# Optimization experiments

Hardware: AMD Instinct MI355X
Metric: run time of the kernel (lower is better)

Reference implementation:

```python
import jax, jax.numpy as jnp
import numpy as np

LEVEL_NUM = 8  # init kwarg level_num (scale is unused by forward)


def setup_inputs() -> dict:
    key = jax.random.key(0)
    x = jax.random.normal(key, (1, 1024, 1024), dtype=jnp.float32)
    return {"x": x}


def reference(x):
    N, H, W = x.shape
    L = LEVEL_NUM
    q_levels = jnp.linspace(x.min(), x.max(), L)          # (L,)
    sigma = 2.0 / L                                        # 1 / (level_num/2)
    # soft quantization: (N,H,W,L)
    quant = jnp.exp(-((x[..., None] - q_levels) ** 2) / (sigma ** 2))
    quant = jnp.transpose(quant, (0, 3, 1, 2))             # (N,L,H,W)
    quant = jnp.pad(quant, ((0, 0), (0, 0), (0, 1), (0, 1)))  # (N,L,H+1,W+1)
    quant_left = quant[:, :, None, :H, :W]                 # (N,L,1,H,W)
    quant_right = quant[:, None, :, 1:, 1:]                # (N,1,L,H,W)
    co_occurrence = quant_left * quant_right               # (N,L,L,H,W)
    sta = co_occurrence.sum(axis=(-1, -2))                 # (N,L,L)
    sta = sta / sta.sum(axis=(1, 2))                       # valid since N==1
    # q_levels_h[n,i,j] = q_levels[j]; q_levels_w[n,i,j] = q_levels[i]
    q_h = jnp.broadcast_to(q_levels[None, None, :], (N, L, L))
    q_w = jnp.broadcast_to(q_levels[None, :, None], (N, L, L))
    output = jnp.stack([q_h, q_w, sta], axis=1).reshape(N, 3, L * L)[0]  # (3, L*L)
    return output, quant[0], co_occurrence[0]
```

## Files before the change

### kernel.cpp

```cpp
#include <hip/hip_runtime.h>

#define H 1024
#define W 1024
#define L 8
#define QH 1025
#define QW 1025
#define OUT0 192
#define QUANT_ELEMS (L * QH * QW)

#define CROWS 32
#define NCHUNK 32
#define BPC 72

#define WS_MIN 0
#define WS_MAX 16
#define WS_STA 32
#define WS_STRIDE 16
#define WS_SLOTS (WS_STA + 64 * WS_STRIDE)

__device__ __forceinline__ unsigned enc_ord(float f) {
    unsigned b = __float_as_uint(f);
    return (b & 0x80000000u) ? ~b : (b ^ 0x80000000u);
}
__device__ __forceinline__ float dec_ord(unsigned u) {
    unsigned b = (u & 0x80000000u) ? (u ^ 0x80000000u) : ~u;
    return __uint_as_float(b);
}
__device__ __forceinline__ float qlev(float mn, float step, float mx, int i) {
    return (i == L - 1) ? mx : mn + step * (float)i;
}

__global__ void k_init(unsigned* ws) {
    int t = threadIdx.x;
    for (int i = t; i < WS_SLOTS; i += 256)
        ws[i] = (i == WS_MIN) ? 0xFFFFFFFFu : 0u;
}

__global__ __launch_bounds__(256) void k_minmax(const float4* __restrict__ x4, unsigned* ws) {
    int t = threadIdx.x;
    int gid = blockIdx.x * 256 + t;
    float mn = 1e30f, mx = -1e30f;
    #pragma unroll
    for (int i = 0; i < 4; ++i) {
        float4 v = x4[gid + i * 65536];
        mn = fminf(mn, fminf(fminf(v.x, v.y), fminf(v.z, v.w)));
        mx = fmaxf(mx, fmaxf(fmaxf(v.x, v.y), fmaxf(v.z, v.w)));
    }
    #pragma unroll
    for (int m = 1; m < 64; m <<= 1) {
        mn = fminf(mn, __shfl_xor(mn, m, 64));
        mx = fmaxf(mx, __shfl_xor(mx, m, 64));
    }
    __shared__ float smn[4], smx[4];
    if ((t & 63) == 0) { smn[t >> 6] = mn; smx[t >> 6] = mx; }
    __syncthreads();
    if (t == 0) {
        mn = fminf(fminf(smn[0], smn[1]), fminf(smn[2], smn[3]));
        mx = fmaxf(fmaxf(smx[0], smx[1]), fmaxf(smx[2], smx[3]));
        atomicMin(&ws[WS_MIN], enc_ord(mn));
        atomicMax(&ws[WS_MAX], enc_ord(mx));
    }
}

__global__ __launch_bounds__(256) void k_main(const float* __restrict__ x,
                                              float* __restrict__ out,
                                              unsigned* __restrict__ ws) {
    const float mnv = dec_ord(ws[WS_MIN]);
    const float mxv = dec_ord(ws[WS_MAX]);
    const float step = (mxv - mnv) * (1.0f / 7.0f);

    float* __restrict__ quant = out + OUT0;
    float* __restrict__ co    = out + OUT0 + QUANT_ELEMS;

    const int bid = blockIdx.x;
    const int c = bid / BPC, k = bid - c * BPC;
    const int r0 = c * CROWS;
    const int t = threadIdx.x, w0 = t * 4;

    if (k < 64) {
        const int i = k >> 3, j = k & 7;
        const float qi = qlev(mnv, step, mxv, i);
        const float qj = qlev(mnv, step, mxv, j);
        float* cop = co + k * (H * W) + r0 * W + w0;
        float acc = 0.0f;

        for (int r = 0; r < CROWS; ++r) {
            const int h = r0 + r;
            float4 xl = *(const float4*)(x + h * W + w0);
            const bool hok = (h + 1 < H);
            float xr0 = 0.f, xr1 = 0.f, xr2 = 0.f, xr3 = 0.f;
            bool ok3 = false;
            if (hok) {
                float4 a = *(const float4*)(x + (h + 1) * W + w0);
                xr0 = a.y; xr1 = a.z; xr2 = a.w;
                ok3 = (w0 + 4 < W);
                if (ok3) xr3 = x[(h + 1) * W + w0 + 4];
            }
            float d;
            d = xl.x - qi; float l0 = __expf(-16.f * d * d);
            d = xl.y - qi; float l1 = __expf(-16.f * d * d);
            d = xl.z - qi; float l2 = __expf(-16.f * d * d);
            d = xl.w - qi; float l3 = __expf(-16.f * d * d);
            d = xr0 - qj; float p0 = hok ? __expf(-16.f * d * d) : 0.f;
            d = xr1 - qj; float p1 = hok ? __expf(-16.f * d * d) : 0.f;
            d = xr2 - qj; float p2 = hok ? __expf(-16.f * d * d) : 0.f;
            d = xr3 - qj; float p3 = (hok && ok3) ? __expf(-16.f * d * d) : 0.f;

            float4 v;
            v.x = l0 * p0; v.y = l1 * p1; v.z = l2 * p2; v.w = l3 * p3;
            *(float4*)cop = v;
            cop += W;
            acc += (v.x + v.y) + (v.z + v.w);
        }

        #pragma unroll
        for (int m = 1; m < 64; m <<= 1) acc += __shfl_xor(acc, m, 64);
        __shared__ float red[4];
        if ((t & 63) == 0) red[t >> 6] = acc;
        __syncthreads();
        if (t == 0)
            atomicAdd((float*)ws + WS_STA + k * WS_STRIDE,
                      (red[0] + red[1]) + (red[2] + red[3]));
    } else {
        const int i = k - 64;
        const float qi = qlev(mnv, step, mxv, i);
        for (int r = 0; r < CROWS; ++r) {
            const int h = r0 + r;
            float4 xl = *(const float4*)(x + h * W + w0);
            float d;
            d = xl.x - qi; float l0 = __expf(-16.f * d * d);
            d = xl.y - qi; float l1 = __expf(-16.f * d * d);
            d = xl.z - qi; float l2 = __expf(-16.f * d * d);
            d = xl.w - qi; float l3 = __expf(-16.f * d * d);
            float* row = quant + (i * QH + h) * QW + w0;
            row[0] = l0; row[1] = l1; row[2] = l2; row[3] = l3;
            if (t == 255) row[4] = 0.0f;
        }
        if (c == NCHUNK - 1) {
            for (int w = t; w < QW; w += 256)
                quant[(i * QH + H) * QW + w] = 0.0f;
        }
    }
}

__global__ void k_final(float* __restrict__ out, const unsigned* __restrict__ ws) {
    int t = threadIdx.x;
    const float mnv = dec_ord(ws[WS_MIN]);
    const float mxv = dec_ord(ws[WS_MAX]);
    const float step = (mxv - mnv) * (1.0f / 7.0f);

    float s = ((const float*)ws)[WS_STA + t * WS_STRIDE];
    float tot = s;
    #pragma unroll
    for (int m = 1; m < 64; m <<= 1) tot += __shfl_xor(tot, m, 64);

    out[t]       = qlev(mnv, step, mxv, t & 7);
    out[64 + t]  = qlev(mnv, step, mxv, t >> 3);
    out[128 + t] = s / tot;
}

extern "C" void kernel_launch(void* const* d_in, const int* in_sizes, int n_in,
                              void* d_out, int out_size, void* d_ws, size_t ws_size,
                              hipStream_t stream) {
    const float* x = (const float*)d_in[0];
    float* out = (float*)d_out;
    unsigned* ws = (unsigned*)d_ws;

    k_init<<<dim3(1), dim3(256), 0, stream>>>(ws);
    k_minmax<<<dim3(256), dim3(256), 0, stream>>>((const float4*)x, ws);
    k_main<<<dim3(NCHUNK * BPC), dim3(256), 0, stream>>>(x, out, ws);
    k_final<<<dim3(1), dim3(64), 0, stream>>>(out, ws);
}
```

Baseline: 72.81 us.

## Drop init kernel and atomics, use nontemporal stores, process three units per block

The k_init kernel is removed. Global atomics for min/max and the co-occurrence sums are replaced by per-block partial slots, which k_main and k_final reduce themselves. Output stores become nontemporal vector stores so the roughly 300MB of writes bypass the cache, and in the co-occurrence loop each row load is carried over to the next iteration instead of being reloaded. Each block now handles three work units, which cuts the grid size but adds extra syncthreads and a redundant partial reduction in every block.

```diff
diff --git a/kernel.cpp b/kernel.cpp
--- a/kernel.cpp
+++ b/kernel.cpp
@@ -11,38 +11,31 @@
 #define CROWS 32
 #define NCHUNK 32
 #define BPC 72
+#define NUNITS (NCHUNK * BPC)
+#define UPB 3
+#define GRID_MAIN (NUNITS / UPB)
 
-#define WS_MIN 0
-#define WS_MAX 16
-#define WS_STA 32
-#define WS_STRIDE 16
-#define WS_SLOTS (WS_STA + 64 * WS_STRIDE)
+#define WS_MINP 0
+#define WS_MAXP 256
+#define WS_STA  512
 
-__device__ __forceinline__ unsigned enc_ord(float f) {
-    unsigned b = __float_as_uint(f);
-    return (b & 0x80000000u) ? ~b : (b ^ 0x80000000u);
-}
-__device__ __forceinline__ float dec_ord(unsigned u) {
-    unsigned b = (u & 0x80000000u) ? (u ^ 0x80000000u) : ~u;
-    return __uint_as_float(b);
+typedef float f32x4 __attribute__((ext_vector_type(4)));
+
+__device__ __forceinline__ void nt_store4(float* p, float a, float b, float c, float d) {
+    f32x4 v = {a, b, c, d};
+    __builtin_nontemporal_store(v, (f32x4*)p);
 }
 __device__ __forceinline__ float qlev(float mn, float step, float mx, int i) {
     return (i == L - 1) ? mx : mn + step * (float)i;
 }
 
-__global__ void k_init(unsigned* ws) {
-    int t = threadIdx.x;
-    for (int i = t; i < WS_SLOTS; i += 256)
-        ws[i] = (i == WS_MIN) ? 0xFFFFFFFFu : 0u;
-}
-
-__global__ __launch_bounds__(256) void k_minmax(const float4* __restrict__ x4, unsigned* ws) {
-    int t = threadIdx.x;
-    int gid = blockIdx.x * 256 + t;
+__global__ __launch_bounds__(256) void k_minmax(const float4* __restrict__ x4,
+                                                float* __restrict__ ws) {
+    const int t = threadIdx.x, b = blockIdx.x;
     float mn = 1e30f, mx = -1e30f;
     #pragma unroll
     for (int i = 0; i < 4; ++i) {
-        float4 v = x4[gid + i * 65536];
+        float4 v = x4[b * 1024 + i * 256 + t];
         mn = fminf(mn, fminf(fminf(v.x, v.y), fminf(v.z, v.w)));
         mx = fmaxf(mx, fmaxf(fmaxf(v.x, v.y), fmaxf(v.z, v.w)));
     }
@@ -55,107 +48,127 @@
     if ((t & 63) == 0) { smn[t >> 6] = mn; smx[t >> 6] = mx; }
     __syncthreads();
     if (t == 0) {
-        mn = fminf(fminf(smn[0], smn[1]), fminf(smn[2], smn[3]));
-        mx = fmaxf(fmaxf(smx[0], smx[1]), fmaxf(smx[2], smx[3]));
-        atomicMin(&ws[WS_MIN], enc_ord(mn));
-        atomicMax(&ws[WS_MAX], enc_ord(mx));
+        ws[WS_MINP + b] = fminf(fminf(smn[0], smn[1]), fminf(smn[2], smn[3]));
+        ws[WS_MAXP + b] = fmaxf(fmaxf(smx[0], smx[1]), fmaxf(smx[2], smx[3]));
     }
 }
 
 __global__ __launch_bounds__(256) void k_main(const float* __restrict__ x,
                                               float* __restrict__ out,
-                                              unsigned* __restrict__ ws) {
-    const float mnv = dec_ord(ws[WS_MIN]);
-    const float mxv = dec_ord(ws[WS_MAX]);
+                                              float* __restrict__ ws) {
+    const int t = threadIdx.x;
+    __shared__ float smn[4], smx[4], red[4];
+
+    float mn = ws[WS_MINP + t], mx = ws[WS_MAXP + t];
+    #pragma unroll
+    for (int m = 1; m < 64; m <<= 1) {
+        mn = fminf(mn, __shfl_xor(mn, m, 64));
+        mx = fmaxf(mx, __shfl_xor(mx, m, 64));
+    }
+    if ((t & 63) == 0) { smn[t >> 6] = mn; smx[t >> 6] = mx; }
+    __syncthreads();
+    const float mnv = fminf(fminf(smn[0], smn[1]), fminf(smn[2], smn[3]));
+    const float mxv = fmaxf(fmaxf(smx[0], smx[1]), fmaxf(smx[2], smx[3]));
     const float step = (mxv - mnv) * (1.0f / 7.0f);
 
     float* __restrict__ quant = out + OUT0;
     float* __restrict__ co    = out + OUT0 + QUANT_ELEMS;
+    const int w0 = t * 4;
+    const bool ok3 = (w0 + 4 < W);
 
-    const int bid = blockIdx.x;
-    const int c = bid / BPC, k = bid - c * BPC;
-    const int r0 = c * CROWS;
-    const int t = threadIdx.x, w0 = t * 4;
+    #pragma unroll
+    for (int uu = 0; uu < UPB; ++uu) {
+        const int u = blockIdx.x * UPB + uu;
+        const int c = u / BPC, k = u - c * BPC;
+        const int r0 = c * CROWS;
 
-    if (k < 64) {
-        const int i = k >> 3, j = k & 7;
-        const float qi = qlev(mnv, step, mxv, i);
-        const float qj = qlev(mnv, step, mxv, j);
-        float* cop = co + k * (H * W) + r0 * W + w0;
-        float acc = 0.0f;
+        if (k < 64) {
+            const float qi = qlev(mnv, step, mxv, k >> 3);
+            const float qj = qlev(mnv, step, mxv, k & 7);
+            float* cop = co + k * (H * W) + r0 * W + w0;
+            float4 cur = *(const float4*)(x + r0 * W + w0);
+            float acc = 0.0f;
 
-        for (int r = 0; r < CROWS; ++r) {
-            const int h = r0 + r;
-            float4 xl = *(const float4*)(x + h * W + w0);
-            const bool hok = (h + 1 < H);
-            float xr0 = 0.f, xr1 = 0.f, xr2 = 0.f, xr3 = 0.f;
-            bool ok3 = false;
-            if (hok) {
-                float4 a = *(const float4*)(x + (h + 1) * W + w0);
-                xr0 = a.y; xr1 = a.z; xr2 = a.w;
-                ok3 = (w0 + 4 < W);
-                if (ok3) xr3 = x[(h + 1) * W + w0 + 4];
+            for (int r = 0; r < CROWS; ++r) {
+                const int h = r0 + r;
+                const bool hok = (h + 1 < H);
+                float4 nxt = make_float4(0.f, 0.f, 0.f, 0.f);
+                float e = 0.f;
+                if (hok) {
+                    nxt = *(const float4*)(x + (h + 1) * W + w0);
+                    if (ok3) e = x[(h + 1) * W + w0 + 4];
+                }
+                float d;
+                d = cur.x - qi; float l0 = __expf(-16.f * d * d);
+                d = cur.y - qi; float l1 = __expf(-16.f * d * d);
+                d = cur.z - qi; float l2 = __expf(-16.f * d * d);
+                d = cur.w - qi; float l3 = __expf(-16.f * d * d);
+                d = nxt.y - qj; float p0 = hok ? __expf(-16.f * d * d) : 0.f;
+                d = nxt.z - qj; float p1 = hok ? __expf(-16.f * d * d) : 0.f;
+                d = nxt.w - qj; float p2 = hok ? __expf(-16.f * d * d) : 0.f;
+                d = e     - qj; float p3 = (hok && ok3) ? __expf(-16.f * d * d) : 0.f;
+
+                float v0 = l0 * p0, v1 = l1 * p1, v2 = l2 * p2, v3 = l3 * p3;
+                nt_store4(cop, v0, v1, v2, v3);
+                cop += W;
+                acc += (v0 + v1) + (v2 + v3);
+                cur = nxt;
             }
-            float d;
-            d = xl.x - qi; float l0 = __expf(-16.f * d * d);
-            d = xl.y - qi; float l1 = __expf(-16.f * d * d);
-            d = xl.z - qi; float l2 = __expf(-16.f * d * d);
-            d = xl.w - qi; float l3 = __expf(-16.f * d * d);
-            d = xr0 - qj; float p0 = hok ? __expf(-16.f * d * d) : 0.f;
-            d = xr1 - qj; float p1 = hok ? __expf(-16.f * d * d) : 0.f;
-            d = xr2 - qj; float p2 = hok ? __expf(-16.f * d * d) : 0.f;
-            d = xr3 - qj; float p3 = (hok && ok3) ? __expf(-16.f * d * d) : 0.f;
 
-            float4 v;
-            v.x = l0 * p0; v.y = l1 * p1; v.z = l2 * p2; v.w = l3 * p3;
-            *(float4*)cop = v;
-            cop += W;
-            acc += (v.x + v.y) + (v.z + v.w);
-        }
-
-        #pragma unroll
-        for (int m = 1; m < 64; m <<= 1) acc += __shfl_xor(acc, m, 64);
-        __shared__ float red[4];
-        if ((t & 63) == 0) red[t >> 6] = acc;
-        __syncthreads();
-        if (t == 0)
-            atomicAdd((float*)ws + WS_STA + k * WS_STRIDE,
-                      (red[0] + red[1]) + (red[2] + red[3]));
-    } else {
-        const int i = k - 64;
-        const float qi = qlev(mnv, step, mxv, i);
-        for (int r = 0; r < CROWS; ++r) {
-            const int h = r0 + r;
-            float4 xl = *(const float4*)(x + h * W + w0);
-            float d;
-            d = xl.x - qi; float l0 = __expf(-16.f * d * d);
-            d = xl.y - qi; float l1 = __expf(-16.f * d * d);
-            d = xl.z - qi; float l2 = __expf(-16.f * d * d);
-            d = xl.w - qi; float l3 = __expf(-16.f * d * d);
-            float* row = quant + (i * QH + h) * QW + w0;
-            row[0] = l0; row[1] = l1; row[2] = l2; row[3] = l3;
-            if (t == 255) row[4] = 0.0f;
-        }
-        if (c == NCHUNK - 1) {
-            for (int w = t; w < QW; w += 256)
-                quant[(i * QH + H) * QW + w] = 0.0f;
+            #pragma unroll
+            for (int m = 1; m < 64; m <<= 1) acc += __shfl_xor(acc, m, 64);
+            __syncthreads();
+            if ((t & 63) == 0) red[t >> 6] = acc;
+            __syncthreads();
+            if (t == 0)
+                ws[WS_STA + c * 64 + k] = (red[0] + red[1]) + (red[2] + red[3]);
+        } else {
+            const int i = k - 64;
+            const float qi = qlev(mnv, step, mxv, i);
+            for (int r = 0; r < CROWS; ++r) {
+                const int h = r0 + r;
+                float4 xl = *(const float4*)(x + h * W + w0);
+                float d;
+                d = xl.x - qi; float l0 = __expf(-16.f * d * d);
+                d = xl.y - qi; float l1 = __expf(-16.f * d * d);
+                d = xl.z - qi; float l2 = __expf(-16.f * d * d);
+                d = xl.w - qi; float l3 = __expf(-16.f * d * d);
+                float* row = quant + (i * QH + h) * QW + w0;
+                nt_store4(row, l0, l1, l2, l3);
+                if (t == 255) __builtin_nontemporal_store(0.f, row + 4);
+            }
+            if (c == NCHUNK - 1) {
+                for (int w = t; w < QW; w += 256)
+                    __builtin_nontemporal_store(0.f, &quant[(i * QH + H) * QW + w]);
+            }
         }
     }
 }
 
-__global__ void k_final(float* __restrict__ out, const unsigned* __restrict__ ws) {
-    int t = threadIdx.x;
-    const float mnv = dec_ord(ws[WS_MIN]);
-    const float mxv = dec_ord(ws[WS_MAX]);
-    const float step = (mxv - mnv) * (1.0f / 7.0f);
+__global__ void k_final(float* __restrict__ out, const float* __restrict__ ws) {
+    const int t = threadIdx.x;
+    float mn = 1e30f, mx = -1e30f;
+    #pragma unroll
+    for (int i = 0; i < 4; ++i) {
+        mn = fminf(mn, ws[WS_MINP + i * 64 + t]);
+        mx = fmaxf(mx, ws[WS_MAXP + i * 64 + t]);
+    }
+    #pragma unroll
+    for (int m = 1; m < 64; m <<= 1) {
+        mn = fminf(mn, __shfl_xor(mn, m, 64));
+        mx = fmaxf(mx, __shfl_xor(mx, m, 64));
+    }
+    const float step = (mx - mn) * (1.0f / 7.0f);
 
-    float s = ((const float*)ws)[WS_STA + t * WS_STRIDE];
+    float s = 0.f;
+    #pragma unroll 8
+    for (int c = 0; c < NCHUNK; ++c) s += ws[WS_STA + c * 64 + t];
     float tot = s;
     #pragma unroll
     for (int m = 1; m < 64; m <<= 1) tot += __shfl_xor(tot, m, 64);
 
-    out[t]       = qlev(mnv, step, mxv, t & 7);
-    out[64 + t]  = qlev(mnv, step, mxv, t >> 3);
+    out[t]       = qlev(mn, step, mx, t & 7);
+    out[64 + t]  = qlev(mn, step, mx, t >> 3);
     out[128 + t] = s / tot;
 }
 
@@ -164,10 +177,9 @@
                               hipStream_t stream) {
     const float* x = (const float*)d_in[0];
     float* out = (float*)d_out;
-    unsigned* ws = (unsigned*)d_ws;
+    float* ws = (float*)d_ws;
 
-    k_init<<<dim3(1), dim3(256), 0, stream>>>(ws);
     k_minmax<<<dim3(256), dim3(256), 0, stream>>>((const float4*)x, ws);
-    k_main<<<dim3(NCHUNK * BPC), dim3(256), 0, stream>>>(x, out, ws);
+    k_main<<<dim3(GRID_MAIN), dim3(256), 0, stream>>>(x, out, ws);
     k_final<<<dim3(1), dim3(64), 0, stream>>>(out, ws);
 }
```

Result: slower. 94.86 us (+30.3%).
